# Performance work log

Measured on AMD Instinct MI355X. Metric: run time of the kernel, lower is better.

## Reference

```python
import jax, jax.numpy as jnp
import numpy as np

B_SZ = 2
D_MODEL = 1024
H = 16
C = 8
BLK = 128
DK = 64
DV = 64
NCHUNK = 1024            # tokens per chunk (divisible by BLK)
T = C * (1 + NCHUNK)     # 8200: [g0, chunk0..., g1, chunk1..., ...]


def setup_inputs() -> dict:
    key = jax.random.key(0)
    k0, k1, k2, k3, k4 = jax.random.split(key, 5)
    s = 0.02
    x  = jax.random.normal(k0, (B_SZ, T, D_MODEL), dtype=jnp.float32)
    Wq = jax.random.normal(k1, (D_MODEL, H * DK), dtype=jnp.float32) * s
    Wk = jax.random.normal(k2, (D_MODEL, H * DK), dtype=jnp.float32) * s
    Wv = jax.random.normal(k3, (D_MODEL, H * DV), dtype=jnp.float32) * s
    Wo = jax.random.normal(k4, (H * DV, D_MODEL), dtype=jnp.float32) * s
    bo = jnp.zeros((D_MODEL,), dtype=jnp.float32)
    return {"x": x, "Wq": Wq, "Wk": Wk, "Wv": Wv, "Wo": Wo, "bo": bo}


def _local_sparse_3block(qf, kf, vf):
    # qf,kf: [BC, H, N, dk], vf: [BC, H, N, dv]; window = [left, current, right] blocks
    bc, h, n, dk = qf.shape
    dv = vf.shape[-1]
    nb = n // BLK
    q = qf.reshape(bc, h, nb, BLK, dk)
    k = kf.reshape(bc, h, nb, BLK, dk)
    v = vf.reshape(bc, h, nb, BLK, dv)
    zk = jnp.zeros((bc, h, 1, BLK, dk), qf.dtype)
    zv = jnp.zeros((bc, h, 1, BLK, dv), qf.dtype)
    kp = jnp.concatenate([zk, k, zk], axis=2)          # [bc,h,nb+2,B,dk]
    vp = jnp.concatenate([zv, v, zv], axis=2)
    k_win = jnp.concatenate([kp[:, :, 0:nb], kp[:, :, 1:nb + 1], kp[:, :, 2:nb + 2]], axis=3)  # [bc,h,nb,3B,dk]
    v_win = jnp.concatenate([vp[:, :, 0:nb], vp[:, :, 1:nb + 1], vp[:, :, 2:nb + 2]], axis=3)  # [bc,h,nb,3B,dv]
    scale = 1.0 / np.sqrt(dk).astype(np.float32)
    scores = jnp.einsum('bhnqd,bhnkd->bhnqk', q, k_win) * scale   # [bc,h,nb,B,3B]
    mask = np.zeros((nb, 3 * BLK), dtype=bool)
    mask[0, :BLK] = True           # first block: left padding invalid
    mask[-1, 2 * BLK:] = True      # last block: right padding invalid
    scores = jnp.where(jnp.asarray(mask)[None, None, :, None, :], -jnp.inf, scores)
    attn = jax.nn.softmax(scores, axis=-1)
    out = jnp.einsum('bhnqk,bhnkd->bhnqd', attn, v_win)
    return out.reshape(bc, h, n, dv)


def reference(x, Wq, Wk, Wv, Wo, bo):
    Bb, Tt, _ = x.shape
    q = (x @ Wq).reshape(Bb, Tt, H, DK).transpose(0, 2, 1, 3)  # [B,H,T,dk]
    k = (x @ Wk).reshape(Bb, Tt, H, DK).transpose(0, 2, 1, 3)
    v = (x @ Wv).reshape(Bb, Tt, H, DV).transpose(0, 2, 1, 3)
    stride = NCHUNK + 1
    g_idx = jnp.arange(C) * stride
    gq = q[:, :, g_idx]  # [B,H,C,dk]
    gk = k[:, :, g_idx]
    gv = v[:, :, g_idx]  # [B,H,C,dv]
    local_idx = ((g_idx + 1)[:, None] + jnp.arange(NCHUNK)[None, :]).reshape(-1)
    qx = q[:, :, local_idx].reshape(Bb, H, C, NCHUNK, DK)
    kx = k[:, :, local_idx].reshape(Bb, H, C, NCHUNK, DK)
    vx = v[:, :, local_idx].reshape(Bb, H, C, NCHUNK, DV)
    # local 3-block attention per chunk
    q_flat = qx.transpose(0, 2, 1, 3, 4).reshape(Bb * C, H, NCHUNK, DK)
    k_flat = kx.transpose(0, 2, 1, 3, 4).reshape(Bb * C, H, NCHUNK, DK)
    v_flat = vx.transpose(0, 2, 1, 3, 4).reshape(Bb * C, H, NCHUNK, DV)
    out_local = _local_sparse_3block(q_flat, k_flat, v_flat)
    out_local = out_local.reshape(Bb, C, H, NCHUNK, DV).transpose(0, 2, 1, 3, 4)  # [B,H,C,Nchunk,dv]
    # each local token additionally receives its chunk's global value directly
    out_chunks = out_local + gv[:, :, :, None, :]
    # global tokens attend over all globals + own chunk's locals (joint softmax, fp32)
    scale = 1.0 / np.sqrt(DK).astype(np.float32)
    scores_gg = jnp.einsum('bhcd,bhed->bhce', gq, gk) * scale      # [B,H,C,C]
    scores_gl = jnp.einsum('bhcd,bhcnd->bhcn', gq, kx) * scale     # [B,H,C,Nchunk]
    attn = jax.nn.softmax(jnp.concatenate([scores_gg, scores_gl], axis=-1), axis=-1)
    a_gg, a_gl = attn[..., :C], attn[..., C:]
    out_g = (jnp.einsum('bhce,bhed->bhcd', a_gg, gv)
             + jnp.einsum('bhcn,bhcnd->bhcd', a_gl, vx))           # [B,H,C,dv]
    out_inter = jnp.concatenate([out_g[:, :, :, None, :], out_chunks], axis=3)  # [B,H,C,1+Nchunk,dv]
    out = out_inter.reshape(Bb, H, Tt, DV).transpose(0, 2, 1, 3).reshape(Bb, Tt, H * DV)
    return out @ Wo + bo
```

## Files before the change

### kernel.cpp

```cpp
#include <hip/hip_runtime.h>
#include <hip/hip_bf16.h>

typedef __bf16 bf16x8 __attribute__((ext_vector_type(8)));
typedef float  f32x4  __attribute__((ext_vector_type(4)));
typedef unsigned short u16x8 __attribute__((ext_vector_type(8)));
typedef unsigned short u16x4 __attribute__((ext_vector_type(4)));

#define T_TOK   8200
#define M_TOK   16400
#define QKV_LD  3072
#define DM      1024

#define AS1CU const __attribute__((address_space(1))) unsigned int*
#define AS3U  __attribute__((address_space(3))) unsigned int*
#define GLDS16(g, s) __builtin_amdgcn_global_load_lds((AS1CU)(g), (AS3U)(s), 16, 0, 0)

__device__ __forceinline__ unsigned short f2bf(float f){
  __hip_bfloat16 h = __float2bfloat16(f);
  return *reinterpret_cast<unsigned short*>(&h);
}
__device__ __forceinline__ float bf2f(unsigned short u){
  union { unsigned u; float f; } x; x.u = ((unsigned)u) << 16;
  return x.f;
}

__global__ void k_cvt(const float* __restrict__ in, unsigned short* __restrict__ out, long n4){
  long i = (long)blockIdx.x * blockDim.x + threadIdx.x;
  long stride = (long)gridDim.x * blockDim.x;
  for (long e = i; e < n4; e += stride){
    float4 v = ((const float4*)in)[e];
    u16x4 o; o[0]=f2bf(v.x); o[1]=f2bf(v.y); o[2]=f2bf(v.z); o[3]=f2bf(v.w);
    ((u16x4*)out)[e] = o;
  }
}

__global__ __launch_bounds__(256) void k_wT4(const float* __restrict__ Wq, const float* __restrict__ Wk,
                                             const float* __restrict__ Wv, const float* __restrict__ Wo,
                                             unsigned short* __restrict__ wqkvt, unsigned short* __restrict__ wot){
  __shared__ float t[64][65];
  const float* W; unsigned short* Wt;
  int z = blockIdx.z;
  if      (z == 0){ W = Wq; Wt = wqkvt; }
  else if (z == 1){ W = Wk; Wt = wqkvt + (size_t)1024*1024; }
  else if (z == 2){ W = Wv; Wt = wqkvt + (size_t)2048*1024; }
  else            { W = Wo; Wt = wot; }
  int tk0 = blockIdx.x * 64, tn0 = blockIdx.y * 64;
  int tid = threadIdx.x;
#pragma unroll
  for (int i = 0; i < 4; i++){
    int ch = tid + i*256; int kr = ch >> 4, n4 = (ch & 15) * 4;
    float4 v = *(const float4*)(W + (size_t)(tk0+kr)*1024 + tn0 + n4);
    t[kr][n4+0]=v.x; t[kr][n4+1]=v.y; t[kr][n4+2]=v.z; t[kr][n4+3]=v.w;
  }
  __syncthreads();
#pragma unroll
  for (int i = 0; i < 4; i++){
    int ch = tid + i*256; int nr = ch >> 4, k4 = (ch & 15) * 4;
    u16x4 o;
#pragma unroll
    for (int e = 0; e < 4; e++) o[e] = f2bf(t[k4+e][nr]);
    *(u16x4*)(Wt + (size_t)(tn0+nr)*1024 + tk0 + k4) = o;
  }
}

__global__ __launch_bounds__(256,2) void k_gemm(const unsigned short* __restrict__ A,
                                                const unsigned short* __restrict__ Bt,
                                                const float* __restrict__ bias,
                                                void* __restrict__ Cout,
                                                int M, int K, int ldc, int bf16out, int gn){
  __shared__ unsigned short As[128][64];
  __shared__ unsigned short Bs[128][64];
  int tid = threadIdx.x, l = tid & 63, w = tid >> 6;
  int li = l & 15, lh = l >> 4;
  int nwg = gridDim.x;
  int wg = (blockIdx.x & 7) * (nwg >> 3) + (blockIdx.x >> 3);
  int m0 = (wg / gn) * 128, n0 = (wg % gn) * 128;
  int wm = (w & 1) * 64, wn = (w >> 1) * 64;
  int lr = l >> 3, lc = l & 7;
  int lsw = li & 7;

  f32x4 acc[4][4];
#pragma unroll
  for (int a = 0; a < 4; a++)
#pragma unroll
    for (int b = 0; b < 4; b++) acc[a][b] = 0.f;

  for (int kt = 0; kt < K; kt += 64){
    __syncthreads();
#pragma unroll
    for (int i = 0; i < 4; i++){
      int r = w*32 + i*8 + lr;
      int colsw = (lc ^ (r & 7)) * 8;
      int rga = m0 + r; if (rga >= M) rga = M - 1;
      GLDS16(A  + (size_t)rga     *K + kt + colsw, &As[w*32 + i*8][0]);
      GLDS16(Bt + (size_t)(n0 + r)*K + kt + colsw, &Bs[w*32 + i*8][0]);
    }
    __syncthreads();
#pragma unroll
    for (int ks = 0; ks < 2; ks++){
      bf16x8 af[4], bfr[4];
#pragma unroll
      for (int mt = 0; mt < 4; mt++)
        af[mt] = *(const bf16x8*)&As[wm + mt*16 + li][((ks*4 + lh) ^ lsw) * 8];
#pragma unroll
      for (int nt = 0; nt < 4; nt++)
        bfr[nt] = *(const bf16x8*)&Bs[wn + nt*16 + li][((ks*4 + lh) ^ lsw) * 8];
#pragma unroll
      for (int mt = 0; mt < 4; mt++)
#pragma unroll
        for (int nt = 0; nt < 4; nt++)
          acc[mt][nt] = __builtin_amdgcn_mfma_f32_16x16x32_bf16(af[mt], bfr[nt], acc[mt][nt], 0, 0, 0);
    }
  }
#pragma unroll
  for (int mt = 0; mt < 4; mt++)
#pragma unroll
    for (int nt = 0; nt < 4; nt++)
#pragma unroll
      for (int r = 0; r < 4; r++){
        int row = m0 + wm + mt*16 + lh*4 + r;
        int col = n0 + wn + nt*16 + li;
        if (row < M){
          float v = acc[mt][nt][r] + (bias ? bias[col] : 0.f);
          if (bf16out) ((unsigned short*)Cout)[(size_t)row*ldc + col] = f2bf(v);
          else         ((float*)Cout)[(size_t)row*ldc + col] = v;
        }
      }
}

__global__ __launch_bounds__(256,3) void k_local(const unsigned short* __restrict__ qkv,
                                                 unsigned short* __restrict__ att){
  __shared__ unsigned short Ks[128][64];
  __shared__ unsigned short Vt[64][136];
  __shared__ unsigned short Pb[4][16][136];

  int tid = threadIdx.x, l = tid & 63, w = tid >> 6;
  int li = l & 15, lh = l >> 4;
  int lr = l >> 3, lc = l & 7;
  int lsw = li & 7;
  int wg = (blockIdx.x & 7) * 256 + (blockIdx.x >> 3);
  int blk = wg & 7, c = (wg >> 3) & 7, h = (wg >> 6) & 15, b = wg >> 10;
  size_t bT = (size_t)b * T_TOK;
  int tokq0 = c*1025 + 1 + blk*128;

  bf16x8 aq[2][2];
#pragma unroll
  for (int tr = 0; tr < 2; tr++)
#pragma unroll
    for (int ks = 0; ks < 2; ks++)
      aq[tr][ks] = *(const bf16x8*)(qkv + (bT + tokq0 + w*32 + tr*16 + li)*QKV_LD + h*64 + ks*32 + lh*8);

  float psum[2][4];
  f32x4 oacc[2][4];
#pragma unroll
  for (int tr = 0; tr < 2; tr++)
#pragma unroll
    for (int r = 0; r < 4; r++) psum[tr][r] = 0.f;
#pragma unroll
  for (int tr = 0; tr < 2; tr++)
#pragma unroll
    for (int ct = 0; ct < 4; ct++) oacc[tr][ct] = 0.f;

  for (int kb = blk-1; kb <= blk+1; ++kb){
    if ((unsigned)kb > 7u) continue;
    int tokk0 = c*1025 + 1 + kb*128;

    u16x8 vlo[2], vhi[2];
#pragma unroll
    for (int i = 0; i < 2; i++){
      int gv = 4*i + w;
      const unsigned short* vp = qkv + (bT + tokk0 + 2*l)*QKV_LD + 2048 + h*64 + gv*8;
      vlo[i] = *(const u16x8*)vp;
      vhi[i] = *(const u16x8*)(vp + QKV_LD);
    }
    __syncthreads();
#pragma unroll
    for (int i = 0; i < 4; i++){
      int r = w*32 + i*8 + lr;
      int colk = (lc ^ (r & 7)) * 8;
      GLDS16(qkv + (bT + tokk0 + r)*QKV_LD + 1024 + h*64 + colk, &Ks[w*32 + i*8][0]);
    }
#pragma unroll
    for (int i = 0; i < 2; i++)
#pragma unroll
      for (int e = 0; e < 8; e++){
        unsigned pk = (unsigned)vlo[i][e] | ((unsigned)vhi[i][e] << 16);
        *(unsigned*)&Vt[(4*i + w)*8 + e][2*l] = pk;
      }
    __syncthreads();

    f32x4 s2[2][8];
#pragma unroll
    for (int tr = 0; tr < 2; tr++)
#pragma unroll
      for (int ct = 0; ct < 8; ct++) s2[tr][ct] = 0.f;
#pragma unroll
    for (int ct = 0; ct < 8; ct++)
#pragma unroll
      for (int ks = 0; ks < 2; ks++){
        bf16x8 kf = *(const bf16x8*)&Ks[ct*16 + li][((ks*4 + lh) ^ lsw) * 8];
        s2[0][ct] = __builtin_amdgcn_mfma_f32_16x16x32_bf16(aq[0][ks], kf, s2[0][ct], 0, 0, 0);
        s2[1][ct] = __builtin_amdgcn_mfma_f32_16x16x32_bf16(aq[1][ks], kf, s2[1][ct], 0, 0, 0);
      }

#pragma unroll
    for (int tr = 0; tr < 2; tr++){
#pragma unroll
      for (int ct = 0; ct < 8; ct++)
#pragma unroll
        for (int r = 0; r < 4; r++){
          float p = __expf(s2[tr][ct][r] * 0.125f);
          s2[tr][ct][r] = p;
          psum[tr][r] += p;
        }
#pragma unroll
      for (int ct = 0; ct < 8; ct++)
#pragma unroll
        for (int r = 0; r < 4; r++)
          Pb[w][lh*4 + r][ct*16 + li] = f2bf(s2[tr][ct][r]);
      bf16x8 pa[4];
#pragma unroll
      for (int ks = 0; ks < 4; ks++)
        pa[ks] = *(const bf16x8*)&Pb[w][li][ks*32 + lh*8];
#pragma unroll
      for (int ct = 0; ct < 4; ct++)
#pragma unroll
        for (int ks = 0; ks < 4; ks++){
          bf16x8 vfr = *(const bf16x8*)&Vt[ct*16 + li][ks*32 + lh*8];
          oacc[tr][ct] = __builtin_amdgcn_mfma_f32_16x16x32_bf16(pa[ks], vfr, oacc[tr][ct], 0, 0, 0);
        }
    }
  }

#pragma unroll
  for (int tr = 0; tr < 2; tr++)
#pragma unroll
    for (int r = 0; r < 4; r++)
#pragma unroll
      for (int mk = 1; mk < 16; mk <<= 1)
        psum[tr][r] += __shfl_xor(psum[tr][r], mk);
  float gvv[4];
#pragma unroll
  for (int ct = 0; ct < 4; ct++)
    gvv[ct] = bf2f(qkv[(bT + c*1025)*QKV_LD + 2048 + h*64 + ct*16 + li]);
#pragma unroll
  for (int tr = 0; tr < 2; tr++)
#pragma unroll
    for (int ct = 0; ct < 4; ct++)
#pragma unroll
      for (int r = 0; r < 4; r++){
        int row = w*32 + tr*16 + lh*4 + r;
        float v = oacc[tr][ct][r] / psum[tr][r] + gvv[ct];
        att[(bT + tokq0 + row)*DM + h*64 + ct*16 + li] = f2bf(v);
      }
}

__global__ __launch_bounds__(256) void k_global(const unsigned short* __restrict__ qkv,
                                                unsigned short* __restrict__ att){
  __shared__ float sc[1032];
  __shared__ float red[256];
  __shared__ float gq_s[64];
  int tid = threadIdx.x, bid = blockIdx.x;
  int c = bid & 7, h = (bid >> 3) & 15, b = bid >> 7;
  size_t bT = (size_t)b * T_TOK;
  size_t grow = bT + (size_t)c*1025;
  if (tid < 64) gq_s[tid] = bf2f(qkv[grow*QKV_LD + h*64 + tid]);
  __syncthreads();
  float lmax = -3e38f;
  for (int idx = tid; idx < 1032; idx += 256){
    size_t krow = (idx < 8) ? (bT + (size_t)idx*1025) : (bT + (size_t)c*1025 + 1 + (idx - 8));
    const unsigned short* kp = qkv + krow*QKV_LD + 1024 + h*64;
    float s = 0.f;
#pragma unroll
    for (int d0 = 0; d0 < 64; d0 += 8){
      u16x8 kv = *(const u16x8*)(kp + d0);
#pragma unroll
      for (int e = 0; e < 8; e++) s += gq_s[d0+e] * bf2f(kv[e]);
    }
    s *= 0.125f;
    sc[idx] = s;
    lmax = fmaxf(lmax, s);
  }
  red[tid] = lmax; __syncthreads();
  for (int st = 128; st > 0; st >>= 1){ if (tid < st) red[tid] = fmaxf(red[tid], red[tid+st]); __syncthreads(); }
  float m = red[0]; __syncthreads();
  float lsum = 0.f;
  for (int idx = tid; idx < 1032; idx += 256){
    float p = __expf(sc[idx] - m); sc[idx] = p; lsum += p;
  }
  red[tid] = lsum; __syncthreads();
  for (int st = 128; st > 0; st >>= 1){ if (tid < st) red[tid] += red[tid+st]; __syncthreads(); }
  float denom = red[0]; __syncthreads();
  int d = tid & 63, part = tid >> 6;
  float acc = 0.f;
  for (int idx = part; idx < 1032; idx += 4){
    size_t krow = (idx < 8) ? (bT + (size_t)idx*1025) : (bT + (size_t)c*1025 + 1 + (idx - 8));
    acc += sc[idx] * bf2f(qkv[krow*QKV_LD + 2048 + h*64 + d]);
  }
  red[tid] = acc; __syncthreads();
  if (tid < 64){
    float o = (red[tid] + red[tid+64] + red[tid+128] + red[tid+192]) / denom;
    att[grow*DM + h*64 + tid] = f2bf(o);
  }
}

extern "C" void kernel_launch(void* const* d_in, const int* in_sizes, int n_in,
                              void* d_out, int out_size, void* d_ws, size_t ws_size,
                              hipStream_t stream) {
  const float* x  = (const float*)d_in[0];
  const float* Wq = (const float*)d_in[1];
  const float* Wk = (const float*)d_in[2];
  const float* Wv = (const float*)d_in[3];
  const float* Wo = (const float*)d_in[4];
  const float* bo = (const float*)d_in[5];
  float* out = (float*)d_out;

  unsigned short* xb    = (unsigned short*)d_ws;
  unsigned short* wqkvt = xb    + (size_t)M_TOK * 1024;
  unsigned short* wot   = wqkvt + (size_t)3072 * 1024;
  unsigned short* qkv   = wot   + (size_t)1024 * 1024;
  unsigned short* att   = qkv   + (size_t)M_TOK * QKV_LD;

  long n4 = (long)M_TOK * 1024 / 4;
  k_cvt<<<2048, 256, 0, stream>>>(x, xb, n4);
  k_wT4<<<dim3(16,16,4), 256, 0, stream>>>(Wq, Wk, Wv, Wo, wqkvt, wot);
  k_gemm<<<dim3(129*24), 256, 0, stream>>>(xb, wqkvt, (const float*)nullptr, (void*)qkv,
                                           M_TOK, 1024, QKV_LD, 1, 24);
  k_local<<<2048, 256, 0, stream>>>(qkv, att);
  k_global<<<256, 256, 0, stream>>>(qkv, att);
  k_gemm<<<dim3(129*8), 256, 0, stream>>>(att, wot, bo, (void*)out,
                                          M_TOK, 1024, DM, 0, 8);
}
```

Baseline: 342.0 us.

## Keep softmax probabilities in registers via transposed QK^T MFMA, drop LDS staging

Result: slower. 490.9 us (+43.5%).

```diff
diff --git a/kernel.cpp b/kernel.cpp
--- a/kernel.cpp
+++ b/kernel.cpp
@@ -128,11 +128,10 @@
       }
 }
 
-__global__ __launch_bounds__(256,3) void k_local(const unsigned short* __restrict__ qkv,
+__global__ __launch_bounds__(256,4) void k_local(const unsigned short* __restrict__ qkv,
                                                  unsigned short* __restrict__ att){
   __shared__ unsigned short Ks[128][64];
   __shared__ unsigned short Vt[64][136];
-  __shared__ unsigned short Pb[4][16][136];
 
   int tid = threadIdx.x, l = tid & 63, w = tid >> 6;
   int li = l & 15, lh = l >> 4;
@@ -150,12 +149,8 @@
     for (int ks = 0; ks < 2; ks++)
       aq[tr][ks] = *(const bf16x8*)(qkv + (bT + tokq0 + w*32 + tr*16 + li)*QKV_LD + h*64 + ks*32 + lh*8);
 
-  float psum[2][4];
+  float psum[2] = {0.f, 0.f};
   f32x4 oacc[2][4];
-#pragma unroll
-  for (int tr = 0; tr < 2; tr++)
-#pragma unroll
-    for (int r = 0; r < 4; r++) psum[tr][r] = 0.f;
 #pragma unroll
   for (int tr = 0; tr < 2; tr++)
 #pragma unroll
@@ -199,46 +194,61 @@
 #pragma unroll
       for (int ks = 0; ks < 2; ks++){
         bf16x8 kf = *(const bf16x8*)&Ks[ct*16 + li][((ks*4 + lh) ^ lsw) * 8];
-        s2[0][ct] = __builtin_amdgcn_mfma_f32_16x16x32_bf16(aq[0][ks], kf, s2[0][ct], 0, 0, 0);
-        s2[1][ct] = __builtin_amdgcn_mfma_f32_16x16x32_bf16(aq[1][ks], kf, s2[1][ct], 0, 0, 0);
+        s2[0][ct] = __builtin_amdgcn_mfma_f32_16x16x32_bf16(kf, aq[0][ks], s2[0][ct], 0, 0, 0);
+        s2[1][ct] = __builtin_amdgcn_mfma_f32_16x16x32_bf16(kf, aq[1][ks], s2[1][ct], 0, 0, 0);
       }
 
 #pragma unroll
     for (int tr = 0; tr < 2; tr++){
-#pragma unroll
-      for (int ct = 0; ct < 8; ct++)
-#pragma unroll
-        for (int r = 0; r < 4; r++){
-          float p = __expf(s2[tr][ct][r] * 0.125f);
-          s2[tr][ct][r] = p;
-          psum[tr][r] += p;
+      unsigned pk01[8], pk23[8];
+#pragma unroll
+      for (int ct = 0; ct < 8; ct++){
+        float p0 = __expf(s2[tr][ct][0] * 0.125f);
+        float p1 = __expf(s2[tr][ct][1] * 0.125f);
+        float p2 = __expf(s2[tr][ct][2] * 0.125f);
+        float p3 = __expf(s2[tr][ct][3] * 0.125f);
+        psum[tr] += (p0 + p1) + (p2 + p3);
+        pk01[ct] = (unsigned)f2bf(p0) | ((unsigned)f2bf(p1) << 16);
+        pk23[ct] = (unsigned)f2bf(p2) | ((unsigned)f2bf(p3) << 16);
+      }
+      bf16x8 pa[4];
+#pragma unroll
+      for (int ks = 0; ks < 4; ks++){
+        union { unsigned u[4]; bf16x8 v; } fr;
+        fr.u[0] = pk01[2*ks];
+        fr.u[1] = pk23[2*ks];
+        fr.u[2] = pk01[2*ks + 1];
+        fr.u[3] = pk23[2*ks + 1];
+        pa[ks] = fr.v;
+      }
+#pragma unroll
+      for (int ct = 0; ct < 4; ct++){
+        const unsigned* vrow = (const unsigned*)&Vt[ct*16 + li][0];
+#pragma unroll
+        for (int ks = 0; ks < 4; ks++){
+          int base = ks*16 + 2*lh;
+          union { unsigned u[4]; bf16x8 v; } vf;
+          vf.u[0] = vrow[base];
+          vf.u[1] = vrow[base + 1];
+          vf.u[2] = vrow[base + 8];
+          vf.u[3] = vrow[base + 9];
+          oacc[tr][ct] = __builtin_amdgcn_mfma_f32_16x16x32_bf16(pa[ks], vf.v, oacc[tr][ct], 0, 0, 0);
         }
-#pragma unroll
-      for (int ct = 0; ct < 8; ct++)
-#pragma unroll
-        for (int r = 0; r < 4; r++)
-          Pb[w][lh*4 + r][ct*16 + li] = f2bf(s2[tr][ct][r]);
-      bf16x8 pa[4];
-#pragma unroll
-      for (int ks = 0; ks < 4; ks++)
-        pa[ks] = *(const bf16x8*)&Pb[w][li][ks*32 + lh*8];
-#pragma unroll
-      for (int ct = 0; ct < 4; ct++)
-#pragma unroll
-        for (int ks = 0; ks < 4; ks++){
-          bf16x8 vfr = *(const bf16x8*)&Vt[ct*16 + li][ks*32 + lh*8];
-          oacc[tr][ct] = __builtin_amdgcn_mfma_f32_16x16x32_bf16(pa[ks], vfr, oacc[tr][ct], 0, 0, 0);
-        }
-    }
-  }
-
+      }
+    }
+  }
+
+#pragma unroll
+  for (int tr = 0; tr < 2; tr++){
+    psum[tr] += __shfl_xor(psum[tr], 16, 64);
+    psum[tr] += __shfl_xor(psum[tr], 32, 64);
+  }
+  float ps[2][4];
 #pragma unroll
   for (int tr = 0; tr < 2; tr++)
 #pragma unroll
     for (int r = 0; r < 4; r++)
-#pragma unroll
-      for (int mk = 1; mk < 16; mk <<= 1)
-        psum[tr][r] += __shfl_xor(psum[tr][r], mk);
+      ps[tr][r] = __shfl(psum[tr], lh*4 + r, 64);
   float gvv[4];
 #pragma unroll
   for (int ct = 0; ct < 4; ct++)
@@ -250,7 +260,7 @@
 #pragma unroll
       for (int r = 0; r < 4; r++){
         int row = w*32 + tr*16 + lh*4 + r;
-        float v = oacc[tr][ct][r] / psum[tr][r] + gvv[ct];
+        float v = oacc[tr][ct][r] / ps[tr][r] + gvv[ct];
         att[(bT + tokq0 + row)*DM + h*64 + ct*16 + li] = f2bf(v);
       }
 }
```
